# Kernel tuning notes

Hardware: AMD Instinct MI355X
Metric: run time of the kernel (lower is better)

## Reference

```python
import jax, jax.numpy as jnp
import numpy as np

POS_LEN = 32  # S = POS_LEN**2 = 1024
NUM_F = 16    # fourier features -> input dim 8*16 = 128
HIDDEN = 256
T = 32        # gab_num_templates


def _offsets(pos_len):
    S = pos_len * pos_len
    s_idx = jnp.arange(S)
    s_r = s_idx // pos_len
    s_c = s_idx % pos_len
    dr = (s_r[:, None] - s_r[None, :]).astype(jnp.float32)
    dc = (s_c[:, None] - s_c[None, :]).astype(jnp.float32)
    return dr, dc


def setup_inputs() -> dict:
    key = jax.random.key(0)
    k1, k2, k3, k4 = jax.random.split(key, 4)
    # learnable freqs: exp(linspace(log(1), log(1/50)))
    freqs = jnp.exp(jnp.linspace(jnp.log(1.0), jnp.log(1.0 / 50.0), NUM_F)).astype(jnp.float32)
    fin = 8 * NUM_F
    W1 = jax.random.normal(k1, (HIDDEN, fin), dtype=jnp.float32) * (1.0 / np.sqrt(fin))
    b1 = jax.random.normal(k2, (HIDDEN,), dtype=jnp.float32) * 0.01
    W2 = jax.random.normal(k3, (T, HIDDEN), dtype=jnp.float32) * (1.0 / np.sqrt(HIDDEN))
    b2 = jax.random.normal(k4, (T,), dtype=jnp.float32) * 0.01
    dr, dc = _offsets(POS_LEN)
    return {"seq_len": POS_LEN * POS_LEN, "freqs": freqs, "W1": W1, "b1": b1,
            "W2": W2, "b2": b2, "dr": dr, "dc": dc}


def _fourier_features(dr, dc, freqs):
    # dr, dc: (S, S); freqs: (F,) -> (S, S, 8F)
    f = freqs[None, None, :]
    a = dr[..., None] * f
    b = dc[..., None] * f
    p = (dr + dc)[..., None] * f
    m = (dr - dc)[..., None] * f
    return jnp.concatenate([jnp.sin(a), jnp.cos(a), jnp.sin(b), jnp.cos(b),
                            jnp.sin(p), jnp.cos(p), jnp.sin(m), jnp.cos(m)], axis=-1)


def reference(seq_len, freqs, W1, b1, W2, b2, dr, dc):
    dr_s = dr[:seq_len, :seq_len]
    dc_s = dc[:seq_len, :seq_len]
    feats = _fourier_features(dr_s, dc_s, freqs)          # (S, S, 8F)
    h = jax.nn.silu(jnp.einsum('ijf,hf->ijh', feats, W1) + b1)  # (S, S, H)
    out = jnp.einsum('ijh,th->ijt', h, W2) + b2            # (S, S, T)
    return out * (1.0 / jnp.sqrt(jnp.float32(T)))
```

## Files before the change

kernel.cpp:

```cpp
#include <hip/hip_runtime.h>
#include <math.h>

#define NUM_F   16
#define FIN     (8 * NUM_F)
#define HIDDEN  256
#define TOUT    32
#define NOFF    63
#define NSUM    125
#define NPAIRS_TBL (NOFF * NOFF)
#define PPB     8
#define NBLK    ((NPAIRS_TBL + PPB - 1) / PPB)
#define PROWS   (NOFF + NOFF + NSUM + NSUM)

__global__ __launch_bounds__(256) void gab_ptab_kernel(
    const float* __restrict__ freqs, const float* __restrict__ W1,
    float* __restrict__ P)
{
    __shared__ float fv[32];
    const int rho = blockIdx.x;
    int grp, val;
    if (rho < NOFF)            { grp = 0; val = rho - 31; }
    else if (rho < 2 * NOFF)   { grp = 1; val = rho - NOFF - 31; }
    else if (rho < 2 * NOFF + NSUM) { grp = 2; val = rho - 2 * NOFF - 62; }
    else                       { grp = 3; val = rho - 2 * NOFF - NSUM - 62; }

    const int t = threadIdx.x;
    if (t < 32) {
        const float arg = (float)val * freqs[t & 15];
        fv[t] = (t < 16) ? sinf(arg) : cosf(arg);
    }
    __syncthreads();

    const float4* __restrict__ w4 = (const float4*)(W1 + t * FIN + grp * 32);
    const float4* f4 = (const float4*)fv;
    float a0 = 0.f, a1 = 0.f, a2 = 0.f, a3 = 0.f;
    #pragma unroll
    for (int k = 0; k < 8; k += 2) {
        const float4 wa = w4[k], wb = w4[k + 1];
        const float4 fa = f4[k], fb = f4[k + 1];
        a0 = fmaf(wa.x, fa.x, a0); a1 = fmaf(wa.y, fa.y, a1);
        a2 = fmaf(wa.z, fa.z, a2); a3 = fmaf(wa.w, fa.w, a3);
        a0 = fmaf(wb.x, fb.x, a0); a1 = fmaf(wb.y, fb.y, a1);
        a2 = fmaf(wb.z, fb.z, a2); a3 = fmaf(wb.w, fb.w, a3);
    }
    P[rho * HIDDEN + t] = (a0 + a1) + (a2 + a3);
}

__global__ __launch_bounds__(256) void gab_table_kernel(
    const float* __restrict__ P, const float* __restrict__ b1,
    const float* __restrict__ W2, const float* __restrict__ b2,
    float* __restrict__ table)
{
    __shared__ float hbuf[HIDDEN];
    __shared__ float part[2][4][33];

    const int t = threadIdx.x;
    const int o = t & 31;
    const int c = t >> 5;

    float4 w2r[8];
    {
        const float4* w2v = (const float4*)(W2 + o * HIDDEN + c * 32);
        #pragma unroll
        for (int k = 0; k < 8; ++k) w2r[k] = w2v[k];
    }
    const float b1t = b1[t];
    const float b2o = b2[o];

    const float* __restrict__ Pa = P;
    const float* __restrict__ Pb = P + NOFF * HIDDEN;
    const float* __restrict__ Pp = P + 2 * NOFF * HIDDEN;
    const float* __restrict__ Pm = P + (2 * NOFF + NSUM) * HIDDEN;

    for (int pp = 0; pp < PPB; ++pp) {
        const int pair = blockIdx.x * PPB + pp;
        if (pair >= NPAIRS_TBL) break;
        const int ia = pair / NOFF;
        const int ib = pair % NOFF;
        const int ip = ia + ib;
        const int im = ia - ib + 62;

        const float pre = Pa[ia * HIDDEN + t] + Pb[ib * HIDDEN + t]
                        + Pp[ip * HIDDEN + t] + Pm[im * HIDDEN + t] + b1t;
        hbuf[t] = pre / (1.0f + expf(-pre));
        __syncthreads();

        const float4* h4 = (const float4*)(&hbuf[c * 32]);
        float s0 = 0.f, s1 = 0.f, s2 = 0.f, s3 = 0.f;
        #pragma unroll
        for (int k = 0; k < 8; k += 2) {
            const float4 ha = h4[k], hb = h4[k + 1];
            s0 = fmaf(w2r[k].x,     ha.x, s0); s1 = fmaf(w2r[k].y,     ha.y, s1);
            s2 = fmaf(w2r[k].z,     ha.z, s2); s3 = fmaf(w2r[k].w,     ha.w, s3);
            s0 = fmaf(w2r[k + 1].x, hb.x, s0); s1 = fmaf(w2r[k + 1].y, hb.y, s1);
            s2 = fmaf(w2r[k + 1].z, hb.z, s2); s3 = fmaf(w2r[k + 1].w, hb.w, s3);
        }
        float s = (s0 + s1) + (s2 + s3);
        s += __shfl_xor(s, 32);
        if ((t & 63) < 32) part[pp & 1][t >> 6][o] = s;
        __syncthreads();

        if (t < TOUT) {
            const float r = part[pp & 1][0][t] + part[pp & 1][1][t]
                          + part[pp & 1][2][t] + part[pp & 1][3][t] + b2o;
            table[pair * TOUT + t] = r * 0.17677669529663687f;
        }
    }
}

__global__ __launch_bounds__(256, 2) void gab_table_fallback(
    const float* __restrict__ freqs,
    const float* __restrict__ W1, const float* __restrict__ b1,
    const float* __restrict__ W2, const float* __restrict__ b2,
    float* __restrict__ table)
{
    __shared__ float feats[FIN];
    __shared__ float hbuf2[HIDDEN];
    __shared__ float part2[4][33];

    const int t = threadIdx.x;
    const int o = t & 31;
    const int c = t >> 5;

    float4 w1r[32];
    {
        const float4* w1v = (const float4*)(W1 + t * FIN);
        #pragma unroll
        for (int k = 0; k < 32; ++k) w1r[k] = w1v[k];
    }
    float4 w2r[8];
    {
        const float4* w2v = (const float4*)(W2 + o * HIDDEN + c * 32);
        #pragma unroll
        for (int k = 0; k < 8; ++k) w2r[k] = w2v[k];
    }
    const float b1t = b1[t];
    const float b2o = b2[o];
    const float myfreq = (t < FIN) ? freqs[t & 15] : 0.0f;

    for (int pp = 0; pp < 8; ++pp) {
        const int pair = blockIdx.x * 8 + pp;
        if (pair >= NPAIRS_TBL) break;
        const float dr = (float)(pair / NOFF - (NOFF / 2));
        const float dc = (float)(pair % NOFF - (NOFF / 2));

        if (t < FIN) {
            const int g = t >> 4;
            float bse;
            switch (g >> 1) {
                case 0:  bse = dr;      break;
                case 1:  bse = dc;      break;
                case 2:  bse = dr + dc; break;
                default: bse = dr - dc; break;
            }
            const float arg = bse * myfreq;
            feats[t] = (g & 1) ? cosf(arg) : sinf(arg);
        }
        __syncthreads();

        float a0 = 0.f, a1 = 0.f, a2 = 0.f, a3 = 0.f;
        const float4* f4 = (const float4*)feats;
        #pragma unroll
        for (int k = 0; k < 32; k += 2) {
            float4 fa = f4[k], fb = f4[k + 1];
            a0 = fmaf(w1r[k].x,     fa.x, a0); a1 = fmaf(w1r[k].y,     fa.y, a1);
            a2 = fmaf(w1r[k].z,     fa.z, a2); a3 = fmaf(w1r[k].w,     fa.w, a3);
            a0 = fmaf(w1r[k + 1].x, fb.x, a0); a1 = fmaf(w1r[k + 1].y, fb.y, a1);
            a2 = fmaf(w1r[k + 1].z, fb.z, a2); a3 = fmaf(w1r[k + 1].w, fb.w, a3);
        }
        const float pre = (a0 + a1) + (a2 + a3) + b1t;
        hbuf2[t] = pre / (1.0f + expf(-pre));
        __syncthreads();

        float s0 = 0.f, s1 = 0.f, s2 = 0.f, s3 = 0.f;
        const float4* h4 = (const float4*)(hbuf2 + c * 32);
        #pragma unroll
        for (int k = 0; k < 8; k += 2) {
            float4 ha = h4[k], hb = h4[k + 1];
            s0 = fmaf(w2r[k].x,     ha.x, s0); s1 = fmaf(w2r[k].y,     ha.y, s1);
            s2 = fmaf(w2r[k].z,     ha.z, s2); s3 = fmaf(w2r[k].w,     ha.w, s3);
            s0 = fmaf(w2r[k + 1].x, hb.x, s0); s1 = fmaf(w2r[k + 1].y, hb.y, s1);
            s2 = fmaf(w2r[k + 1].z, hb.z, s2); s3 = fmaf(w2r[k + 1].w, hb.w, s3);
        }
        float s = (s0 + s1) + (s2 + s3);
        s += __shfl_xor(s, 32);
        if ((t & 63) < 32) part2[t >> 6][o] = s;
        __syncthreads();
        if (t < TOUT) {
            const float r = part2[0][t] + part2[1][t] + part2[2][t] + part2[3][t] + b2o;
            table[pair * TOUT + t] = r * 0.17677669529663687f;
        }
        __syncthreads();
    }
}

__global__ __launch_bounds__(256) void gab_gather_kernel(
    const float* __restrict__ table,
    float4* __restrict__ out, int npairs)
{
    const int total = npairs * 8;
    const int stride = gridDim.x * blockDim.x;
    const float4* __restrict__ tbl4 = (const float4*)table;

    for (int idx = blockIdx.x * blockDim.x + threadIdx.x; idx < total; idx += stride) {
        const int p = idx >> 3;
        const int l = idx & 7;
        const int i = p >> 10;
        const int j = p & 1023;
        const int ir = (i >> 5) - (j >> 5) + (NOFF / 2);
        const int ic = (i & 31) - (j & 31) + (NOFF / 2);
        out[idx] = tbl4[(ir * NOFF + ic) * (TOUT / 4) + l];
    }
}

extern "C" void kernel_launch(void* const* d_in, const int* in_sizes, int n_in,
                              void* d_out, int out_size, void* d_ws, size_t ws_size,
                              hipStream_t stream) {
    const float* freqs = (const float*)d_in[1];
    const float* W1    = (const float*)d_in[2];
    const float* b1    = (const float*)d_in[3];
    const float* W2    = (const float*)d_in[4];
    const float* b2    = (const float*)d_in[5];
    float* out = (float*)d_out;

    const int npairs = in_sizes[6];

    const size_t TBL_B = (size_t)NPAIRS_TBL * TOUT * 4;
    const size_t P_B   = (size_t)PROWS * HIDDEN * 4;
    float* table = (float*)d_ws;

    if (ws_size >= TBL_B + P_B) {
        float* P = (float*)((char*)d_ws + TBL_B);
        gab_ptab_kernel <<<PROWS, 256, 0, stream>>>(freqs, W1, P);
        gab_table_kernel<<<NBLK, 256, 0, stream>>>(P, b1, W2, b2, table);
    } else {
        gab_table_fallback<<<(NPAIRS_TBL + 7) / 8, 256, 0, stream>>>(freqs, W1, b1, W2, b2, table);
    }

    gab_gather_kernel<<<2048, 256, 0, stream>>>(table, (float4*)out, npairs);
}
```

Baseline: 41.55 us.

## Restructure table kernel to one wavefront per pair with butterfly reduction

The P-table kernel now computes 8 rows per block, keeping the W1 slice in registers, and launches 48 blocks instead of 376. The table kernel maps each offset pair to one 64-lane wavefront. Each lane handles 4 hidden units with float4 loads and reduces the 32 outputs through a transpose-style shuffle butterfly, which removes the shared-memory buffers and block-wide barriers. The gather kernel, which writes the large output, is unchanged, so the overall gain is limited by that kernel.

```diff
diff --git a/kernel.cpp b/kernel.cpp
--- a/kernel.cpp
+++ b/kernel.cpp
@@ -8,42 +8,61 @@
 #define NOFF    63
 #define NSUM    125
 #define NPAIRS_TBL (NOFF * NOFF)
-#define PPB     8
-#define NBLK    ((NPAIRS_TBL + PPB - 1) / PPB)
 #define PROWS   (NOFF + NOFF + NSUM + NSUM)
 
 __global__ __launch_bounds__(256) void gab_ptab_kernel(
     const float* __restrict__ freqs, const float* __restrict__ W1,
     float* __restrict__ P)
 {
-    __shared__ float fv[32];
-    const int rho = blockIdx.x;
-    int grp, val;
-    if (rho < NOFF)            { grp = 0; val = rho - 31; }
-    else if (rho < 2 * NOFF)   { grp = 1; val = rho - NOFF - 31; }
-    else if (rho < 2 * NOFF + NSUM) { grp = 2; val = rho - 2 * NOFF - 62; }
-    else                       { grp = 3; val = rho - 2 * NOFF - NSUM - 62; }
+    __shared__ float fv_all[8][32];
+
+    const int b = blockIdx.x;
+    int g, c;
+    if (b < 8)       { g = 0; c = b; }
+    else if (b < 16) { g = 1; c = b - 8; }
+    else if (b < 32) { g = 2; c = b - 16; }
+    else             { g = 3; c = b - 32; }
+    const int nrows   = (g < 2) ? NOFF : NSUM;
+    const int rowbase = (g == 0) ? 0 : (g == 1) ? NOFF
+                      : (g == 2) ? 2 * NOFF : 2 * NOFF + NSUM;
+    const int voff    = (g < 2) ? 31 : 62;
 
     const int t = threadIdx.x;
-    if (t < 32) {
-        const float arg = (float)val * freqs[t & 15];
-        fv[t] = (t < 16) ? sinf(arg) : cosf(arg);
+
+    {
+        const int r  = t >> 5;
+        const int e  = t & 31;
+        const int gr = c * 8 + r;
+        if (gr < nrows) {
+            const float arg = (float)(gr - voff) * freqs[e & 15];
+            fv_all[r][e] = (e < 16) ? sinf(arg) : cosf(arg);
+        }
+    }
+
+    float4 w1c[8];
+    {
+        const float4* w4 = (const float4*)(W1 + t * FIN + g * 32);
+        #pragma unroll
+        for (int k = 0; k < 8; ++k) w1c[k] = w4[k];
     }
     __syncthreads();
 
-    const float4* __restrict__ w4 = (const float4*)(W1 + t * FIN + grp * 32);
-    const float4* f4 = (const float4*)fv;
-    float a0 = 0.f, a1 = 0.f, a2 = 0.f, a3 = 0.f;
-    #pragma unroll
-    for (int k = 0; k < 8; k += 2) {
-        const float4 wa = w4[k], wb = w4[k + 1];
-        const float4 fa = f4[k], fb = f4[k + 1];
-        a0 = fmaf(wa.x, fa.x, a0); a1 = fmaf(wa.y, fa.y, a1);
-        a2 = fmaf(wa.z, fa.z, a2); a3 = fmaf(wa.w, fa.w, a3);
-        a0 = fmaf(wb.x, fb.x, a0); a1 = fmaf(wb.y, fb.y, a1);
-        a2 = fmaf(wb.z, fb.z, a2); a3 = fmaf(wb.w, fb.w, a3);
-    }
-    P[rho * HIDDEN + t] = (a0 + a1) + (a2 + a3);
+    #pragma unroll
+    for (int r = 0; r < 8; ++r) {
+        const int gr = c * 8 + r;
+        if (gr >= nrows) break;
+        const float4* f4 = (const float4*)fv_all[r];
+        float a0 = 0.f, a1 = 0.f, a2 = 0.f, a3 = 0.f;
+        #pragma unroll
+        for (int k = 0; k < 8; k += 2) {
+            const float4 fa = f4[k], fb = f4[k + 1];
+            a0 = fmaf(w1c[k].x,     fa.x, a0); a1 = fmaf(w1c[k].y,     fa.y, a1);
+            a2 = fmaf(w1c[k].z,     fa.z, a2); a3 = fmaf(w1c[k].w,     fa.w, a3);
+            a0 = fmaf(w1c[k + 1].x, fb.x, a0); a1 = fmaf(w1c[k + 1].y, fb.y, a1);
+            a2 = fmaf(w1c[k + 1].z, fb.z, a2); a3 = fmaf(w1c[k + 1].w, fb.w, a3);
+        }
+        P[(rowbase + gr) * HIDDEN + t] = (a0 + a1) + (a2 + a3);
+    }
 }
 
 __global__ __launch_bounds__(256) void gab_table_kernel(
@@ -51,60 +70,74 @@
     const float* __restrict__ W2, const float* __restrict__ b2,
     float* __restrict__ table)
 {
-    __shared__ float hbuf[HIDDEN];
-    __shared__ float part[2][4][33];
-
-    const int t = threadIdx.x;
-    const int o = t & 31;
-    const int c = t >> 5;
-
-    float4 w2r[8];
-    {
-        const float4* w2v = (const float4*)(W2 + o * HIDDEN + c * 32);
-        #pragma unroll
-        for (int k = 0; k < 8; ++k) w2r[k] = w2v[k];
-    }
-    const float b1t = b1[t];
-    const float b2o = b2[o];
-
-    const float* __restrict__ Pa = P;
-    const float* __restrict__ Pb = P + NOFF * HIDDEN;
-    const float* __restrict__ Pp = P + 2 * NOFF * HIDDEN;
-    const float* __restrict__ Pm = P + (2 * NOFF + NSUM) * HIDDEN;
-
-    for (int pp = 0; pp < PPB; ++pp) {
-        const int pair = blockIdx.x * PPB + pp;
-        if (pair >= NPAIRS_TBL) break;
-        const int ia = pair / NOFF;
-        const int ib = pair % NOFF;
-        const int ip = ia + ib;
-        const int im = ia - ib + 62;
-
-        const float pre = Pa[ia * HIDDEN + t] + Pb[ib * HIDDEN + t]
-                        + Pp[ip * HIDDEN + t] + Pm[im * HIDDEN + t] + b1t;
-        hbuf[t] = pre / (1.0f + expf(-pre));
-        __syncthreads();
-
-        const float4* h4 = (const float4*)(&hbuf[c * 32]);
-        float s0 = 0.f, s1 = 0.f, s2 = 0.f, s3 = 0.f;
-        #pragma unroll
-        for (int k = 0; k < 8; k += 2) {
-            const float4 ha = h4[k], hb = h4[k + 1];
-            s0 = fmaf(w2r[k].x,     ha.x, s0); s1 = fmaf(w2r[k].y,     ha.y, s1);
-            s2 = fmaf(w2r[k].z,     ha.z, s2); s3 = fmaf(w2r[k].w,     ha.w, s3);
-            s0 = fmaf(w2r[k + 1].x, hb.x, s0); s1 = fmaf(w2r[k + 1].y, hb.y, s1);
-            s2 = fmaf(w2r[k + 1].z, hb.z, s2); s3 = fmaf(w2r[k + 1].w, hb.w, s3);
-        }
-        float s = (s0 + s1) + (s2 + s3);
-        s += __shfl_xor(s, 32);
-        if ((t & 63) < 32) part[pp & 1][t >> 6][o] = s;
-        __syncthreads();
-
-        if (t < TOUT) {
-            const float r = part[pp & 1][0][t] + part[pp & 1][1][t]
-                          + part[pp & 1][2][t] + part[pp & 1][3][t] + b2o;
-            table[pair * TOUT + t] = r * 0.17677669529663687f;
-        }
+    const int pair = blockIdx.x * 4 + (threadIdx.x >> 6);
+    if (pair >= NPAIRS_TBL) return;
+    const int l = threadIdx.x & 63;
+
+    const int ia = pair / NOFF;
+    const int ib = pair % NOFF;
+    const int ip = ia + ib;
+    const int im = ia - ib + 62;
+
+    const float4* __restrict__ P4 = (const float4*)P;
+    const float4 pa = P4[(0 * NOFF              + ia) * 64 + l];
+    const float4 pb = P4[(1 * NOFF              + ib) * 64 + l];
+    const float4 pp = P4[(2 * NOFF              + ip) * 64 + l];
+    const float4 pm = P4[((2 * NOFF + NSUM)     + im) * 64 + l];
+    const float4 bb = ((const float4*)b1)[l];
+
+    float h0 = pa.x + pb.x + pp.x + pm.x + bb.x;
+    float h1 = pa.y + pb.y + pp.y + pm.y + bb.y;
+    float h2 = pa.z + pb.z + pp.z + pm.z + bb.z;
+    float h3 = pa.w + pb.w + pp.w + pm.w + bb.w;
+    h0 = h0 / (1.0f + expf(-h0));
+    h1 = h1 / (1.0f + expf(-h1));
+    h2 = h2 / (1.0f + expf(-h2));
+    h3 = h3 / (1.0f + expf(-h3));
+
+    float acc[32];
+    const float4* __restrict__ W24 = (const float4*)W2;
+    #pragma unroll
+    for (int o = 0; o < 32; ++o) {
+        const float4 w = W24[o * 64 + l];
+        acc[o] = fmaf(w.x, h0, fmaf(w.y, h1, fmaf(w.z, h2, w.w * h3)));
+    }
+
+    #pragma unroll
+    for (int i = 0; i < 16; ++i) {
+        const float keep = (l & 1) ? acc[i + 16] : acc[i];
+        const float send = (l & 1) ? acc[i] : acc[i + 16];
+        acc[i] = keep + __shfl_xor(send, 1);
+    }
+    #pragma unroll
+    for (int i = 0; i < 8; ++i) {
+        const float keep = (l & 2) ? acc[i + 8] : acc[i];
+        const float send = (l & 2) ? acc[i] : acc[i + 8];
+        acc[i] = keep + __shfl_xor(send, 2);
+    }
+    #pragma unroll
+    for (int i = 0; i < 4; ++i) {
+        const float keep = (l & 4) ? acc[i + 4] : acc[i];
+        const float send = (l & 4) ? acc[i] : acc[i + 4];
+        acc[i] = keep + __shfl_xor(send, 4);
+    }
+    #pragma unroll
+    for (int i = 0; i < 2; ++i) {
+        const float keep = (l & 8) ? acc[i + 2] : acc[i];
+        const float send = (l & 8) ? acc[i] : acc[i + 2];
+        acc[i] = keep + __shfl_xor(send, 8);
+    }
+    {
+        const float keep = (l & 16) ? acc[1] : acc[0];
+        const float send = (l & 16) ? acc[0] : acc[1];
+        acc[0] = keep + __shfl_xor(send, 16);
+    }
+    const float tot = acc[0] + __shfl_xor(acc[0], 32);
+
+    if (l < 32) {
+        const int o = ((l & 1) << 4) | ((l & 2) << 2) | (l & 4)
+                    | ((l & 8) >> 2) | ((l & 16) >> 4);
+        table[pair * TOUT + o] = (tot + b2[o]) * 0.17677669529663687f;
     }
 }
 
@@ -231,8 +264,8 @@
 
     if (ws_size >= TBL_B + P_B) {
         float* P = (float*)((char*)d_ws + TBL_B);
-        gab_ptab_kernel <<<PROWS, 256, 0, stream>>>(freqs, W1, P);
-        gab_table_kernel<<<NBLK, 256, 0, stream>>>(P, b1, W2, b2, table);
+        gab_ptab_kernel <<<48, 256, 0, stream>>>(freqs, W1, P);
+        gab_table_kernel<<<(NPAIRS_TBL + 3) / 4, 256, 0, stream>>>(P, b1, W2, b2, table);
     } else {
         gab_table_fallback<<<(NPAIRS_TBL + 7) / 8, 256, 0, stream>>>(freqs, W1, b1, W2, b2, table);
     }
```

New measurement: 40.16 us. 3.4% less time.
